# Performance work log

Hardware: AMD Instinct MI355X
Metric: run time of the kernel (lower is better)

The kernel has to match this reference:

```python
import jax, jax.numpy as jnp
import numpy as np

BS, E = 32, 4096  # BS fixed by repeat_interleave(32) in the source


def setup_inputs() -> dict:
    key = jax.random.key(0)
    ks = jax.random.split(key, 8)
    s = lambda k, shape, scale=0.02: jax.random.normal(k, shape, dtype=jnp.float32) * scale
    return {
        "image_features": jax.random.normal(ks[0], (BS, E), dtype=jnp.float32),
        "text_features": jax.random.normal(ks[1], (BS, E), dtype=jnp.float32),
        # fusion: BN(2E) -> ReLU -> Linear(2E,E)
        "fs_bn_g": jnp.ones((2 * E,), jnp.float32),
        "fs_bn_b": jnp.zeros((2 * E,), jnp.float32),
        "fs_w": s(ks[2], (2 * E, E)),
        "fs_b": jnp.zeros((E,), jnp.float32),
        # gating: Linear(E,E) -> BN -> ReLU -> Linear(E,E) -> Sigmoid
        "gt_w1": s(ks[3], (E, E)),
        "gt_b1": jnp.zeros((E,), jnp.float32),
        "gt_bn_g": jnp.ones((E,), jnp.float32),
        "gt_bn_b": jnp.zeros((E,), jnp.float32),
        "gt_w2": s(ks[4], (E, E)),
        "gt_b2": jnp.zeros((E,), jnp.float32),
        # 3 error-encoding blocks: Linear(E,E/2)->BN->ReLU->Linear(E/2,E)+residual
        "ee_w1": s(ks[5], (3, E, E // 2)),
        "ee_b1": jnp.zeros((3, E // 2), jnp.float32),
        "ee_bn_g": jnp.ones((3, E // 2), jnp.float32),
        "ee_bn_b": jnp.zeros((3, E // 2), jnp.float32),
        "ee_w2": s(ks[6], (3, E // 2, E)),
        "ee_b2": jnp.zeros((3, E), jnp.float32),
        "cell_id": 1,
    }


def _bn(x, g, b, eps=1e-5):
    # training-mode BatchNorm1d: per-call batch statistics (biased variance)
    mu = jnp.mean(x, axis=0, keepdims=True)
    var = jnp.mean((x - mu) ** 2, axis=0, keepdims=True)
    return (x - mu) * jax.lax.rsqrt(var + eps) * g + b


def reference(image_features, text_features, fs_bn_g, fs_bn_b, fs_w, fs_b,
              gt_w1, gt_b1, gt_bn_g, gt_bn_b, gt_w2, gt_b2,
              ee_w1, ee_b1, ee_bn_g, ee_bn_b, ee_w2, ee_b2, cell_id):
    # cell_id != 0 branch: the per-sample Python loop is vectorized with vmap.
    def compose(txt_row):  # txt_row: [E] -> tiled to [BS, E] (repeat_interleave of [1,E])
        t = jnp.broadcast_to(txt_row[None, :], image_features.shape)
        x = jnp.concatenate([image_features, t], axis=1)          # [BS, 2E]
        f = jax.nn.relu(_bn(x, fs_bn_g, fs_bn_b)) @ fs_w + fs_b   # fusion -> [BS, E]
        g = jax.nn.sigmoid(
            jax.nn.relu(_bn(f @ gt_w1 + gt_b1, gt_bn_g, gt_bn_b)) @ gt_w2 + gt_b2
        )                                                          # gating -> [BS, E]
        ff = f
        for i in range(3):  # structurally distinct error-encoding blocks
            h = jax.nn.relu(_bn(ff @ ee_w1[i] + ee_b1[i], ee_bn_g[i], ee_bn_b[i]))
            ff = h @ ee_w2[i] + ee_b2[i] + ff                      # residual
        return image_features * g + ff * (1.0 - g)                # [BS, E]

    return jax.vmap(compose)(text_features)                        # [BS, BS, E]
```

## Files before the change

### kernel.cpp

```cpp
#include <hip/hip_runtime.h>
#include <math.h>

#define EDIM 4096
#define BS 32
#define NT 64
#define KSPLIT 4
#define NWAVES 4
#define BLK 256

__device__ __forceinline__ float relu_f(float x) { return x > 0.f ? x : 0.f; }

__global__ void __launch_bounds__(BLK) prep_kernel(
    const float* __restrict__ img, const float* __restrict__ bng,
    const float* __restrict__ bnb, float* __restrict__ act0,
    float* __restrict__ vvec, int* __restrict__ flag)
{
  int n = blockIdx.x * BLK + threadIdx.x;
  float bv = bnb[EDIM + n];
  float vv = relu_f(bv);
  vvec[n] = vv;
  if (vv != 0.f) atomicOr(flag, 1);

  float s = 0.f, s2 = 0.f;
  for (int r = 0; r < BS; ++r) {
    float x = img[(size_t)r * EDIM + n];
    s += x; s2 += x * x;
  }
  float mean = s * (1.f / BS);
  float var  = s2 * (1.f / BS) - mean * mean;
  float sc = bng[n] * rsqrtf(var + 1e-5f);
  float sh = bnb[n] - mean * sc;
  for (int r = 0; r < BS; ++r) {
    float x = img[(size_t)r * EDIM + n];
    act0[(size_t)n * BS + r] = relu_f(x * sc + sh);
  }
}

__global__ void __launch_bounds__(BLK) mm_stage(
    const float* __restrict__ W, const float* __restrict__ Ain,
    const float* __restrict__ bias,
    const float* __restrict__ bng, const float* __restrict__ bnb,
    const float* __restrict__ res,
    const float* __restrict__ Wlow, const float* __restrict__ vvec,
    const int* __restrict__ flag,
    float* __restrict__ acc, int* __restrict__ counter,
    float* __restrict__ dst,
    int K, int N, int mode)
{
  const int tid  = threadIdx.x;
  const int bx   = blockIdx.x;
  const int tile = bx >> 2;
  const int ks   = bx & (KSPLIT - 1);
  const int wv   = __builtin_amdgcn_readfirstlane(tid >> 6);
  const int lane = tid & 63;
  const int n    = tile * NT + lane;
  const int kchunk = K / (KSPLIT * NWAVES);
  const int k0     = (ks * NWAVES + wv) * kchunk;

  float racc[BS];
#pragma unroll
  for (int r = 0; r < BS; ++r) racc[r] = 0.f;

  const float* wp = W + (size_t)k0 * N + n;
  const float* ap = Ain + (size_t)k0 * BS;

#pragma unroll 4
  for (int k = 0; k < kchunk; ++k) {
    float wval = wp[(size_t)k * N];
    const float* arow = ap + (size_t)k * BS;
#pragma unroll
    for (int r = 0; r < BS; ++r) racc[r] = fmaf(arow[r], wval, racc[r]);
  }

  if (Wlow != nullptr) {
    if (*flag) {
      float cpart = 0.f;
      const float* wl = Wlow + (size_t)k0 * N + n;
      for (int k = 0; k < kchunk; ++k)
        cpart = fmaf(vvec[k0 + k], wl[(size_t)k * N], cpart);
#pragma unroll
      for (int r = 0; r < BS; ++r) racc[r] += cpart;
    }
  }

  __shared__ float sred[NWAVES][NT][BS];
#pragma unroll
  for (int r = 0; r < BS; r += 4)
    *(float4*)&sred[wv][lane][r] = make_float4(racc[r], racc[r+1], racc[r+2], racc[r+3]);
  __syncthreads();

  const int c  = tid >> 2;
  const int rb = (tid & 3) * 8;
  float tot[8];
#pragma unroll
  for (int u = 0; u < 8; ++u)
    tot[u] = sred[0][c][rb+u] + sred[1][c][rb+u] + sred[2][c][rb+u] + sred[3][c][rb+u];

  const int col = tile * NT + c;
  float* ga = acc + (size_t)col * BS + rb;
#pragma unroll
  for (int u = 0; u < 8; ++u) atomicAdd(ga + u, tot[u]);

  __threadfence();
  __syncthreads();
  __shared__ int s_last;
  if (tid == 0) {
    int old = atomicAdd(counter + tile, 1);
    s_last = (old == KSPLIT - 1) ? 1 : 0;
  }
  __syncthreads();
  if (!s_last) return;

  float val[8];
#pragma unroll
  for (int u = 0; u < 8; ++u)
    val[u] = __hip_atomic_load(ga + u, __ATOMIC_RELAXED, __HIP_MEMORY_SCOPE_AGENT);

  const float bb = bias[col];
#pragma unroll
  for (int u = 0; u < 8; ++u) val[u] += bb;

  if (mode == 1) {
    __shared__ float sps[NT][4], sps2[NT][4], ssc[NT], ssh[NT];
    float p = 0.f, p2 = 0.f;
#pragma unroll
    for (int u = 0; u < 8; ++u) { p += val[u]; p2 += val[u] * val[u]; }
    sps[c][tid & 3] = p; sps2[c][tid & 3] = p2;
    __syncthreads();
    if (tid < NT) {
      float s  = sps[tid][0] + sps[tid][1] + sps[tid][2] + sps[tid][3];
      float s2 = sps2[tid][0] + sps2[tid][1] + sps2[tid][2] + sps2[tid][3];
      float mean = s * (1.f / BS);
      float var  = s2 * (1.f / BS) - mean * mean;
      float sc = bng[tile * NT + tid] * rsqrtf(var + 1e-5f);
      ssc[tid] = sc;
      ssh[tid] = bnb[tile * NT + tid] - mean * sc;
    }
    __syncthreads();
    float sc = ssc[c], sh = ssh[c];
    float* dp = dst + (size_t)col * BS + rb;
#pragma unroll
    for (int u = 0; u < 8; ++u) dp[u] = relu_f(val[u] * sc + sh);
  } else if (mode == 2) {
#pragma unroll
    for (int u = 0; u < 8; ++u) {
      float g = 1.f / (1.f + __expf(-val[u]));
      dst[(size_t)(rb + u) * EDIM + col] = g;
    }
  } else if (mode == 3) {
    const float* rp = res + (size_t)col * BS + rb;
    float* dp = dst + (size_t)col * BS + rb;
#pragma unroll
    for (int u = 0; u < 8; ++u) dp[u] = val[u] + rp[u];
  } else {
    float* dp = dst + (size_t)col * BS + rb;
#pragma unroll
    for (int u = 0; u < 8; ++u) dp[u] = val[u];
  }
}

__global__ void __launch_bounds__(BLK) final_kernel(
    const float* __restrict__ img, const float* __restrict__ grm,
    const float* __restrict__ fft, float* __restrict__ out)
{
  __shared__ float sff[BS][NT];
  const int tid  = threadIdx.x;
  const int tile = blockIdx.x & 63;
  const int jg   = blockIdx.x >> 6;
  const int c  = tid >> 2;
  const int rb = (tid & 3) * 8;
  const float* src = fft + (size_t)(tile * NT + c) * BS + rb;
#pragma unroll
  for (int u = 0; u < 8; ++u) sff[rb + u][c] = src[u];
  __syncthreads();

  const int le = tid & 63, rg = tid >> 6;
  const int e  = tile * NT + le;
#pragma unroll
  for (int rr = 0; rr < 8; ++rr) {
    int r = rr * 4 + rg;
    float gv = grm[(size_t)r * EDIM + e];
    float iv = img[(size_t)r * EDIM + e];
    float o  = iv * gv + sff[r][le] * (1.f - gv);
#pragma unroll
    for (int jj = 0; jj < 8; ++jj) {
      int j = jg * 8 + jj;
      out[((size_t)(j * BS + r)) * EDIM + e] = o;
    }
  }
}

extern "C" void kernel_launch(void* const* d_in, const int* in_sizes, int n_in,
                              void* d_out, int out_size, void* d_ws, size_t ws_size,
                              hipStream_t stream)
{
  const float* img    = (const float*)d_in[0];
  const float* fs_bng = (const float*)d_in[2];
  const float* fs_bnb = (const float*)d_in[3];
  const float* fs_w   = (const float*)d_in[4];
  const float* fs_b   = (const float*)d_in[5];
  const float* gt_w1  = (const float*)d_in[6];
  const float* gt_b1  = (const float*)d_in[7];
  const float* gt_bng = (const float*)d_in[8];
  const float* gt_bnb = (const float*)d_in[9];
  const float* gt_w2  = (const float*)d_in[10];
  const float* gt_b2  = (const float*)d_in[11];
  const float* ee_w1  = (const float*)d_in[12];
  const float* ee_b1  = (const float*)d_in[13];
  const float* ee_bng = (const float*)d_in[14];
  const float* ee_bnb = (const float*)d_in[15];
  const float* ee_w2  = (const float*)d_in[16];
  const float* ee_b2  = (const float*)d_in[17];
  float* out = (float*)d_out;

  float* w = (float*)d_ws;
  size_t o = 0;
  float* acc_fs = w + o; o += (size_t)EDIM * BS;
  float* acc_g1 = w + o; o += (size_t)EDIM * BS;
  float* acc_g2 = w + o; o += (size_t)EDIM * BS;
  float* acc_ea[3]; for (int i = 0; i < 3; ++i) { acc_ea[i] = w + o; o += (size_t)(EDIM/2) * BS; }
  float* acc_eb[3]; for (int i = 0; i < 3; ++i) { acc_eb[i] = w + o; o += (size_t)EDIM * BS; }
  int* counters = (int*)(w + o); o += 1024;
  int* flag = counters + 960;
  size_t zero_bytes = o * sizeof(float);
  float* act0 = w + o; o += (size_t)EDIM * BS;
  float* vvec = w + o; o += EDIM;
  float* fbuf = w + o; o += (size_t)EDIM * BS;
  float* hgb  = w + o; o += (size_t)EDIM * BS;
  float* gbuf = w + o; o += (size_t)EDIM * BS;
  float* he[3];  for (int i = 0; i < 3; ++i) { he[i]  = w + o; o += (size_t)(EDIM/2) * BS; }
  float* ffb[3]; for (int i = 0; i < 3; ++i) { ffb[i] = w + o; o += (size_t)EDIM * BS; }

  hipMemsetAsync(d_ws, 0, zero_bytes, stream);

  prep_kernel<<<EDIM / BLK, BLK, 0, stream>>>(img, fs_bng, fs_bnb, act0, vvec, flag);

  mm_stage<<<(EDIM / NT) * KSPLIT, BLK, 0, stream>>>(
      fs_w, act0, fs_b, nullptr, nullptr, nullptr,
      fs_w + (size_t)EDIM * EDIM, vvec, flag,
      acc_fs, counters + 0, fbuf, EDIM, EDIM, 0);

  mm_stage<<<(EDIM / NT) * KSPLIT, BLK, 0, stream>>>(
      gt_w1, fbuf, gt_b1, gt_bng, gt_bnb, nullptr, nullptr, nullptr, nullptr,
      acc_g1, counters + 64, hgb, EDIM, EDIM, 1);
  mm_stage<<<(EDIM / NT) * KSPLIT, BLK, 0, stream>>>(
      gt_w2, hgb, gt_b2, nullptr, nullptr, nullptr, nullptr, nullptr, nullptr,
      acc_g2, counters + 128, gbuf, EDIM, EDIM, 2);

  const float* ffin = fbuf;
  for (int i = 0; i < 3; ++i) {
    mm_stage<<<((EDIM / 2) / NT) * KSPLIT, BLK, 0, stream>>>(
        ee_w1 + (size_t)i * EDIM * (EDIM / 2), ffin,
        ee_b1 + (size_t)i * (EDIM / 2), ee_bng + (size_t)i * (EDIM / 2),
        ee_bnb + (size_t)i * (EDIM / 2),
        nullptr, nullptr, nullptr, nullptr,
        acc_ea[i], counters + 192 + i * 128, he[i], EDIM, EDIM / 2, 1);
    mm_stage<<<(EDIM / NT) * KSPLIT, BLK, 0, stream>>>(
        ee_w2 + (size_t)i * (EDIM / 2) * EDIM, he[i],
        ee_b2 + (size_t)i * EDIM, nullptr, nullptr, ffin,
        nullptr, nullptr, nullptr,
        acc_eb[i], counters + 256 + i * 128, ffb[i], EDIM / 2, EDIM, 3);
    ffin = ffb[i];
  }

  final_kernel<<<64 * 4, BLK, 0, stream>>>(img, gbuf, ffin, out);
}
```

Before: 886.9 us.

## Widen GEMM column tile to two columns per lane and raise split-K factor

Each lane of the matmul stage now computes two output columns, loading weights as float2 and activations as float4, so every activation load feeds twice as many FMAs. The split-K factor becomes a runtime shift (16 or 32 groups instead of 4), which keeps or raises the block count on the machine and gives each wave a shorter K chunk. The shared reduction buffer is padded and read with vector loads. The prep kernel is also rewritten so four row-groups per block reduce BN statistics through shared memory instead of one thread looping over all rows. The cost is doubled accumulator registers per thread (hence launch_bounds with 2 blocks) and more global atomics per output from the larger split-K.

Measured after the change: 1.764 ms. 1.99x slower.

```diff
diff --git a/kernel.cpp b/kernel.cpp
--- a/kernel.cpp
+++ b/kernel.cpp
@@ -4,7 +4,7 @@
 #define EDIM 4096
 #define BS 32
 #define NT 64
-#define KSPLIT 4
+#define NT2 128
 #define NWAVES 4
 #define BLK 256
 
@@ -15,28 +15,45 @@
     const float* __restrict__ bnb, float* __restrict__ act0,
     float* __restrict__ vvec, int* __restrict__ flag)
 {
-  int n = blockIdx.x * BLK + threadIdx.x;
-  float bv = bnb[EDIM + n];
-  float vv = relu_f(bv);
-  vvec[n] = vv;
-  if (vv != 0.f) atomicOr(flag, 1);
-
+  __shared__ float ss[64][5], ss2[64][5];
+  __shared__ float ssc[64], ssh[64];
+  const int tid = threadIdx.x;
+  const int c  = tid & 63;
+  const int rg = tid >> 6;
+  const int n  = blockIdx.x * 64 + c;
+
+  float xv[8];
   float s = 0.f, s2 = 0.f;
-  for (int r = 0; r < BS; ++r) {
-    float x = img[(size_t)r * EDIM + n];
-    s += x; s2 += x * x;
-  }
-  float mean = s * (1.f / BS);
-  float var  = s2 * (1.f / BS) - mean * mean;
-  float sc = bng[n] * rsqrtf(var + 1e-5f);
-  float sh = bnb[n] - mean * sc;
-  for (int r = 0; r < BS; ++r) {
-    float x = img[(size_t)r * EDIM + n];
-    act0[(size_t)n * BS + r] = relu_f(x * sc + sh);
-  }
+#pragma unroll
+  for (int u = 0; u < 8; ++u) {
+    float x = img[(size_t)(rg * 8 + u) * EDIM + n];
+    xv[u] = x; s += x; s2 += x * x;
+  }
+  ss[c][rg] = s; ss2[c][rg] = s2;
+  __syncthreads();
+
+  if (tid < 64) {
+    float S  = ss[tid][0] + ss[tid][1] + ss[tid][2] + ss[tid][3];
+    float S2 = ss2[tid][0] + ss2[tid][1] + ss2[tid][2] + ss2[tid][3];
+    float mean = S * (1.f / BS);
+    float var  = S2 * (1.f / BS) - mean * mean;
+    int nn = blockIdx.x * 64 + tid;
+    float sc = bng[nn] * rsqrtf(var + 1e-5f);
+    ssc[tid] = sc;
+    ssh[tid] = bnb[nn] - mean * sc;
+    float vv = relu_f(bnb[EDIM + nn]);
+    vvec[nn] = vv;
+    if (vv != 0.f) atomicOr(flag, 1);
+  }
+  __syncthreads();
+
+  const float sc = ssc[c], sh = ssh[c];
+#pragma unroll
+  for (int u = 0; u < 8; ++u)
+    act0[(size_t)n * BS + rg * 8 + u] = relu_f(xv[u] * sc + sh);
 }
 
-__global__ void __launch_bounds__(BLK) mm_stage(
+__global__ void __launch_bounds__(BLK, 2) mm_stage(
     const float* __restrict__ W, const float* __restrict__ Ain,
     const float* __restrict__ bias,
     const float* __restrict__ bng, const float* __restrict__ bnb,
@@ -45,105 +62,128 @@
     const int* __restrict__ flag,
     float* __restrict__ acc, int* __restrict__ counter,
     float* __restrict__ dst,
-    int K, int N, int mode)
+    int K, int N, int kgShift, int mode)
 {
   const int tid  = threadIdx.x;
   const int bx   = blockIdx.x;
-  const int tile = bx >> 2;
-  const int ks   = bx & (KSPLIT - 1);
+  const int KG   = 1 << kgShift;
+  const int tile = bx >> kgShift;
+  const int ks   = bx & (KG - 1);
   const int wv   = __builtin_amdgcn_readfirstlane(tid >> 6);
   const int lane = tid & 63;
-  const int n    = tile * NT + lane;
-  const int kchunk = K / (KSPLIT * NWAVES);
+  const int n0   = tile * NT2 + lane * 2;
+  const int kchunk = K >> (kgShift + 2);
   const int k0     = (ks * NWAVES + wv) * kchunk;
 
-  float racc[BS];
-#pragma unroll
-  for (int r = 0; r < BS; ++r) racc[r] = 0.f;
-
-  const float* wp = W + (size_t)k0 * N + n;
-  const float* ap = Ain + (size_t)k0 * BS;
+  float r0[BS], r1[BS];
+#pragma unroll
+  for (int r = 0; r < BS; ++r) { r0[r] = 0.f; r1[r] = 0.f; }
+
+  const float* __restrict__ wp = W + (size_t)k0 * N + n0;
+  const float* __restrict__ ap = Ain + (size_t)k0 * BS;
 
 #pragma unroll 4
   for (int k = 0; k < kchunk; ++k) {
-    float wval = wp[(size_t)k * N];
-    const float* arow = ap + (size_t)k * BS;
-#pragma unroll
-    for (int r = 0; r < BS; ++r) racc[r] = fmaf(arow[r], wval, racc[r]);
+    const float2 w2 = *(const float2*)(wp + (size_t)k * N);
+    const float* __restrict__ arow = ap + (size_t)k * BS;
+#pragma unroll
+    for (int q = 0; q < 8; ++q) {
+      const float4 a4 = *(const float4*)(arow + (q << 2));
+      const int b = q << 2;
+      r0[b+0] = fmaf(a4.x, w2.x, r0[b+0]);  r1[b+0] = fmaf(a4.x, w2.y, r1[b+0]);
+      r0[b+1] = fmaf(a4.y, w2.x, r0[b+1]);  r1[b+1] = fmaf(a4.y, w2.y, r1[b+1]);
+      r0[b+2] = fmaf(a4.z, w2.x, r0[b+2]);  r1[b+2] = fmaf(a4.z, w2.y, r1[b+2]);
+      r0[b+3] = fmaf(a4.w, w2.x, r0[b+3]);  r1[b+3] = fmaf(a4.w, w2.y, r1[b+3]);
+    }
   }
 
   if (Wlow != nullptr) {
     if (*flag) {
-      float cpart = 0.f;
-      const float* wl = Wlow + (size_t)k0 * N + n;
-      for (int k = 0; k < kchunk; ++k)
-        cpart = fmaf(vvec[k0 + k], wl[(size_t)k * N], cpart);
-#pragma unroll
-      for (int r = 0; r < BS; ++r) racc[r] += cpart;
-    }
-  }
-
-  __shared__ float sred[NWAVES][NT][BS];
-#pragma unroll
-  for (int r = 0; r < BS; r += 4)
-    *(float4*)&sred[wv][lane][r] = make_float4(racc[r], racc[r+1], racc[r+2], racc[r+3]);
-  __syncthreads();
-
-  const int c  = tid >> 2;
-  const int rb = (tid & 3) * 8;
-  float tot[8];
-#pragma unroll
-  for (int u = 0; u < 8; ++u)
-    tot[u] = sred[0][c][rb+u] + sred[1][c][rb+u] + sred[2][c][rb+u] + sred[3][c][rb+u];
-
-  const int col = tile * NT + c;
+      float c0 = 0.f, c1 = 0.f;
+      const float* __restrict__ wl = Wlow + (size_t)k0 * N + n0;
+#pragma unroll 4
+      for (int k = 0; k < kchunk; ++k) {
+        const float2 w2 = *(const float2*)(wl + (size_t)k * N);
+        const float vvk = vvec[k0 + k];
+        c0 = fmaf(vvk, w2.x, c0);
+        c1 = fmaf(vvk, w2.y, c1);
+      }
+#pragma unroll
+      for (int r = 0; r < BS; ++r) { r0[r] += c0; r1[r] += c1; }
+    }
+  }
+
+  __shared__ float sred[NWAVES][NT2][BS + 4];
+#pragma unroll
+  for (int r = 0; r < BS; r += 4) {
+    *(float4*)&sred[wv][lane * 2 + 0][r] = make_float4(r0[r], r0[r+1], r0[r+2], r0[r+3]);
+    *(float4*)&sred[wv][lane * 2 + 1][r] = make_float4(r1[r], r1[r+1], r1[r+2], r1[r+3]);
+  }
+  __syncthreads();
+
+  const int c  = tid >> 1;
+  const int rb = (tid & 1) * 16;
+  float tot[16];
+#pragma unroll
+  for (int u = 0; u < 16; u += 4) {
+    float4 t0 = *(const float4*)&sred[0][c][rb + u];
+    float4 t1 = *(const float4*)&sred[1][c][rb + u];
+    float4 t2 = *(const float4*)&sred[2][c][rb + u];
+    float4 t3 = *(const float4*)&sred[3][c][rb + u];
+    tot[u+0] = t0.x + t1.x + t2.x + t3.x;
+    tot[u+1] = t0.y + t1.y + t2.y + t3.y;
+    tot[u+2] = t0.z + t1.z + t2.z + t3.z;
+    tot[u+3] = t0.w + t1.w + t2.w + t3.w;
+  }
+
+  const int col = tile * NT2 + c;
   float* ga = acc + (size_t)col * BS + rb;
 #pragma unroll
-  for (int u = 0; u < 8; ++u) atomicAdd(ga + u, tot[u]);
+  for (int u = 0; u < 16; ++u) atomicAdd(ga + u, tot[u]);
 
   __threadfence();
   __syncthreads();
   __shared__ int s_last;
   if (tid == 0) {
     int old = atomicAdd(counter + tile, 1);
-    s_last = (old == KSPLIT - 1) ? 1 : 0;
+    s_last = (old == KG - 1) ? 1 : 0;
   }
   __syncthreads();
   if (!s_last) return;
 
-  float val[8];
-#pragma unroll
-  for (int u = 0; u < 8; ++u)
+  float val[16];
+#pragma unroll
+  for (int u = 0; u < 16; ++u)
     val[u] = __hip_atomic_load(ga + u, __ATOMIC_RELAXED, __HIP_MEMORY_SCOPE_AGENT);
 
   const float bb = bias[col];
 #pragma unroll
-  for (int u = 0; u < 8; ++u) val[u] += bb;
+  for (int u = 0; u < 16; ++u) val[u] += bb;
 
   if (mode == 1) {
-    __shared__ float sps[NT][4], sps2[NT][4], ssc[NT], ssh[NT];
+    __shared__ float sps[NT2][2], sps2[NT2][2], ssc[NT2], ssh[NT2];
     float p = 0.f, p2 = 0.f;
 #pragma unroll
-    for (int u = 0; u < 8; ++u) { p += val[u]; p2 += val[u] * val[u]; }
-    sps[c][tid & 3] = p; sps2[c][tid & 3] = p2;
+    for (int u = 0; u < 16; ++u) { p += val[u]; p2 += val[u] * val[u]; }
+    sps[c][tid & 1] = p; sps2[c][tid & 1] = p2;
     __syncthreads();
-    if (tid < NT) {
-      float s  = sps[tid][0] + sps[tid][1] + sps[tid][2] + sps[tid][3];
-      float s2 = sps2[tid][0] + sps2[tid][1] + sps2[tid][2] + sps2[tid][3];
+    if (tid < NT2) {
+      float s  = sps[tid][0] + sps[tid][1];
+      float s2 = sps2[tid][0] + sps2[tid][1];
       float mean = s * (1.f / BS);
       float var  = s2 * (1.f / BS) - mean * mean;
-      float sc = bng[tile * NT + tid] * rsqrtf(var + 1e-5f);
+      float sc = bng[tile * NT2 + tid] * rsqrtf(var + 1e-5f);
       ssc[tid] = sc;
-      ssh[tid] = bnb[tile * NT + tid] - mean * sc;
+      ssh[tid] = bnb[tile * NT2 + tid] - mean * sc;
     }
     __syncthreads();
     float sc = ssc[c], sh = ssh[c];
     float* dp = dst + (size_t)col * BS + rb;
 #pragma unroll
-    for (int u = 0; u < 8; ++u) dp[u] = relu_f(val[u] * sc + sh);
+    for (int u = 0; u < 16; ++u) dp[u] = relu_f(val[u] * sc + sh);
   } else if (mode == 2) {
 #pragma unroll
-    for (int u = 0; u < 8; ++u) {
+    for (int u = 0; u < 16; ++u) {
       float g = 1.f / (1.f + __expf(-val[u]));
       dst[(size_t)(rb + u) * EDIM + col] = g;
     }
@@ -151,11 +191,11 @@
     const float* rp = res + (size_t)col * BS + rb;
     float* dp = dst + (size_t)col * BS + rb;
 #pragma unroll
-    for (int u = 0; u < 8; ++u) dp[u] = val[u] + rp[u];
+    for (int u = 0; u < 16; ++u) dp[u] = val[u] + rp[u];
   } else {
     float* dp = dst + (size_t)col * BS + rb;
 #pragma unroll
-    for (int u = 0; u < 8; ++u) dp[u] = val[u];
+    for (int u = 0; u < 16; ++u) dp[u] = val[u];
   }
 }
 
@@ -233,33 +273,33 @@
 
   hipMemsetAsync(d_ws, 0, zero_bytes, stream);
 
-  prep_kernel<<<EDIM / BLK, BLK, 0, stream>>>(img, fs_bng, fs_bnb, act0, vvec, flag);
-
-  mm_stage<<<(EDIM / NT) * KSPLIT, BLK, 0, stream>>>(
+  prep_kernel<<<EDIM / 64, BLK, 0, stream>>>(img, fs_bng, fs_bnb, act0, vvec, flag);
+
+  mm_stage<<<(EDIM / NT2) * 16, BLK, 0, stream>>>(
       fs_w, act0, fs_b, nullptr, nullptr, nullptr,
       fs_w + (size_t)EDIM * EDIM, vvec, flag,
-      acc_fs, counters + 0, fbuf, EDIM, EDIM, 0);
-
-  mm_stage<<<(EDIM / NT) * KSPLIT, BLK, 0, stream>>>(
+      acc_fs, counters + 0, fbuf, EDIM, EDIM, 4, 0);
+
+  mm_stage<<<(EDIM / NT2) * 16, BLK, 0, stream>>>(
       gt_w1, fbuf, gt_b1, gt_bng, gt_bnb, nullptr, nullptr, nullptr, nullptr,
-      acc_g1, counters + 64, hgb, EDIM, EDIM, 1);
-  mm_stage<<<(EDIM / NT) * KSPLIT, BLK, 0, stream>>>(
+      acc_g1, counters + 64, hgb, EDIM, EDIM, 4, 1);
+  mm_stage<<<(EDIM / NT2) * 16, BLK, 0, stream>>>(
       gt_w2, hgb, gt_b2, nullptr, nullptr, nullptr, nullptr, nullptr, nullptr,
-      acc_g2, counters + 128, gbuf, EDIM, EDIM, 2);
+      acc_g2, counters + 128, gbuf, EDIM, EDIM, 4, 2);
 
   const float* ffin = fbuf;
   for (int i = 0; i < 3; ++i) {
-    mm_stage<<<((EDIM / 2) / NT) * KSPLIT, BLK, 0, stream>>>(
+    mm_stage<<<((EDIM / 2) / NT2) * 32, BLK, 0, stream>>>(
         ee_w1 + (size_t)i * EDIM * (EDIM / 2), ffin,
         ee_b1 + (size_t)i * (EDIM / 2), ee_bng + (size_t)i * (EDIM / 2),
         ee_bnb + (size_t)i * (EDIM / 2),
         nullptr, nullptr, nullptr, nullptr,
-        acc_ea[i], counters + 192 + i * 128, he[i], EDIM, EDIM / 2, 1);
-    mm_stage<<<(EDIM / NT) * KSPLIT, BLK, 0, stream>>>(
+        acc_ea[i], counters + 192 + i * 128, he[i], EDIM, EDIM / 2, 5, 1);
+    mm_stage<<<(EDIM / NT2) * 16, BLK, 0, stream>>>(
         ee_w2 + (size_t)i * (EDIM / 2) * EDIM, he[i],
         ee_b2 + (size_t)i * EDIM, nullptr, nullptr, ffin,
         nullptr, nullptr, nullptr,
-        acc_eb[i], counters + 256 + i * 128, ffb[i], EDIM / 2, EDIM, 3);
+        acc_eb[i], counters + 256 + i * 128, ffb[i], EDIM / 2, EDIM, 4, 3);
     ffin = ffb[i];
   }
 
```
